# Performance work log

Hardware: AMD Instinct MI355X
Metric: run time of the kernel (lower is better)

The kernel has to match this reference:

```python
import jax, jax.numpy as jnp
import numpy as np
import math

HEADS = 8
KSIZE = 25  # decomposition moving-average window

def moving_avg(x, k):
    # x: [B, S, E]; replicate-pad last axis by (k-1)//2 on both sides, window mean (stride 1)
    p = (k - 1) // 2
    xp = jnp.pad(x, ((0, 0), (0, 0), (p, p)), mode='edge')
    cs = jnp.cumsum(xp, axis=-1)
    cs = jnp.concatenate([jnp.zeros_like(cs[..., :1]), cs], axis=-1)
    return (cs[..., k:] - cs[..., :-k]) / k

def decompose(x, k):
    trend = moving_avg(x, k)
    return x - trend, trend

def setup_inputs() -> dict:
    key = jax.random.key(0)
    ks = jax.random.split(key, 16)
    B, S, E = 4, 2048, 256
    H = HEADS
    D = E // H
    FF = 4 * E
    OUT = E
    s = 0.02
    inp = {
        'x': jax.random.normal(ks[0], (B, S, E), dtype=jnp.float32),
        'mask': jnp.ones((B, 1, 1, S), dtype=jnp.int32),
        'wq': jax.random.normal(ks[1], (D, D), dtype=jnp.float32) * s,
        'wk': jax.random.normal(ks[2], (D, D), dtype=jnp.float32) * s,
        'wv': jax.random.normal(ks[3], (D, D), dtype=jnp.float32) * s,
        'w_out': jax.random.normal(ks[4], (E, E), dtype=jnp.float32) * s,
        'b_out': jnp.zeros((E,), dtype=jnp.float32),
        'ff_w1': jax.random.normal(ks[5], (E, FF), dtype=jnp.float32) * s,
        'ff_b1': jnp.zeros((FF,), dtype=jnp.float32),
        'ff_w2': jax.random.normal(ks[6], (FF, E), dtype=jnp.float32) * s,
        'ff_b2': jnp.zeros((E,), dtype=jnp.float32),
        'pr_w1': jax.random.normal(ks[7], (E, FF), dtype=jnp.float32) * s,
        'pr_b1': jnp.zeros((FF,), dtype=jnp.float32),
        'pr_w2': jax.random.normal(ks[8], (FF, OUT), dtype=jnp.float32) * s,
        'pr_b2': jnp.zeros((OUT,), dtype=jnp.float32),
    }
    return inp

def reference(x, mask, wq, wk, wv, w_out, b_out, ff_w1, ff_b1, ff_w2, ff_b2, pr_w1, pr_b1, pr_w2, pr_b2):
    B, S, E = x.shape
    H = HEADS
    D = E // H
    # multihead attention (per-head shared projections, scale by sqrt(embed_size))
    xh = x.reshape(B, S, H, D)
    q = xh @ wq
    k = xh @ wk
    v = xh @ wv
    scores = jnp.einsum('nqhd,nkhd->nhqk', q, k) / jnp.float32(math.sqrt(E))
    scores = jnp.where(mask == 0, jnp.float32(-1e20), scores)
    attn = jax.nn.softmax(scores, axis=-1)
    attn_out = jnp.einsum('nhqk,nkhd->nqhd', attn, v).reshape(B, S, E)
    attn_out = attn_out @ w_out + b_out
    # residual (dropout is identity at inference)
    x = x + attn_out
    # first decomposition: keep seasonal part
    y, _ = decompose(x, KSIZE)
    # FFN
    z = jnp.maximum(y @ ff_w1 + ff_b1, 0.0) @ ff_w2 + ff_b2
    s = y + z
    # second decomposition
    s, _ = decompose(s, KSIZE)
    # projection FFN
    out = jnp.maximum(s @ pr_w1 + pr_b1, 0.0) @ pr_w2 + pr_b2
    return out
```

## Files before the change

kernel.cpp:

```cpp
#include <hip/hip_runtime.h>
#include <hip/hip_bf16.h>
#include <math.h>

#define B_   4
#define S_   2048
#define E_   256
#define H_   8
#define D_   32
#define FF_  1024
#define NTOK (B_*S_)

typedef __attribute__((ext_vector_type(8))) short short8;
typedef __attribute__((ext_vector_type(4))) float f32x4;
typedef __attribute__((ext_vector_type(4))) unsigned u32x4;
typedef __hip_bfloat16 bf16;

#define QSCALE 0.09016844005556021f

__device__ __forceinline__ unsigned short round_bf16(float a) {
    unsigned ua = __builtin_bit_cast(unsigned, a);
    return (unsigned short)((ua + 0x7fffu + ((ua >> 16) & 1u)) >> 16);
}
__device__ __forceinline__ unsigned cvtpk_bf16(float lo, float hi) {
    unsigned r;
    asm("v_cvt_pk_bf16_f32 %0, %1, %2" : "=v"(r) : "v"(lo), "v"(hi));
    return r;
}
__device__ __forceinline__ float fexp2(float x) {
    float r;
    asm("v_exp_f32 %0, %1" : "=v"(r) : "v"(x));
    return r;
}
__device__ __forceinline__ void gld16(const short* g, short* l) {
    __builtin_amdgcn_global_load_lds(
        (const __attribute__((address_space(1))) unsigned int*)g,
        (__attribute__((address_space(3))) unsigned int*)l, 16, 0, 0);
}
__device__ __forceinline__ short8 lds_frag(const short* base, int r, int c16) {
    return *(const short8*)(base + r*64 + (((c16) ^ (r & 7)) << 3));
}

__global__ __launch_bounds__(256) void qkv_prep_kernel(
    const float* __restrict__ x,
    const float* __restrict__ wq, const float* __restrict__ wk, const float* __restrict__ wv,
    bf16* __restrict__ q, bf16* __restrict__ k, bf16* __restrict__ v,
    const float* __restrict__ w_out, const float* __restrict__ ff_w1,
    const float* __restrict__ ff_w2, const float* __restrict__ pr_w1,
    const float* __restrict__ pr_w2,
    unsigned short* __restrict__ woT, unsigned short* __restrict__ f1T,
    unsigned short* __restrict__ f2T, unsigned short* __restrict__ p1T,
    unsigned short* __restrict__ p2T,
    const int* __restrict__ mask, int* __restrict__ mflags)
{
    const int bid = blockIdx.x;
    if (bid >= 512) {
        const int pb = bid - 512;
        if (pb >= 1088) {
            const int t = threadIdx.x;
            if (t < 128) {
                const int* p = mask + (t >> 5)*S_ + (t & 31)*64;
                int any0 = 0;
                #pragma unroll
                for (int i = 0; i < 16; ++i) {
                    const int4 vv = *(const int4*)(p + i*4);
                    if (!(vv.x && vv.y && vv.z && vv.w)) any0 = 1;
                }
                mflags[t] = any0;
            }
            return;
        }
        const float* w; unsigned short* wt; int K, N, idx;
        if (pb < 64)       { w = w_out; wt = woT; K = E_;  N = E_;  idx = pb; }
        else if (pb < 320) { w = ff_w1; wt = f1T; K = E_;  N = FF_; idx = pb - 64; }
        else if (pb < 576) { w = ff_w2; wt = f2T; K = FF_; N = E_;  idx = pb - 320; }
        else if (pb < 832) { w = pr_w1; wt = p1T; K = E_;  N = FF_; idx = pb - 576; }
        else               { w = pr_w2; wt = p2T; K = FF_; N = E_;  idx = pb - 832; }
        const int nb = N/32;
        const int n0 = (idx % nb)*32, k0 = (idx / nb)*32;
        __shared__ float tile[32][33];
        const int c = threadIdx.x & 31, r0 = threadIdx.x >> 5;
        #pragma unroll
        for (int i = 0; i < 4; ++i)
            tile[r0 + 8*i][c] = w[(size_t)(k0 + r0 + 8*i)*N + n0 + c];
        __syncthreads();
        #pragma unroll
        for (int i = 0; i < 4; ++i)
            wt[(size_t)(n0 + r0 + 8*i)*K + k0 + c] = round_bf16(tile[c][r0 + 8*i]);
        return;
    }
    __shared__ float wqs[D_*D_], wks[D_*D_], wvs[D_*D_];
    __shared__ float xs[16][E_];
    const int tid = threadIdx.x;
    for (int i = tid; i < D_*D_; i += 256) {
        wqs[i] = wq[i]; wks[i] = wk[i]; wvs[i] = wv[i];
    }
    const int tok0 = bid * 16;
    #pragma unroll
    for (int i = 0; i < 16; ++i)
        xs[i][tid] = x[(size_t)(tok0 + i)*E_ + tid];
    __syncthreads();
    const int h = tid >> 5, d = tid & 31;
    for (int t = 0; t < 16; ++t) {
        float aq = 0.f, ak = 0.f, av = 0.f;
        #pragma unroll
        for (int i = 0; i < D_; ++i) {
            const float xv = xs[t][h*D_ + i];
            aq += xv * wqs[i*D_ + d];
            ak += xv * wks[i*D_ + d];
            av += xv * wvs[i*D_ + d];
        }
        const int tok = tok0 + t;
        const int b = tok >> 11;
        const int s = tok & (S_-1);
        const int u = s & 63;
        const int sp = (s & ~63) | (((u>>5)&1)*32 + ((u>>2)&1)*16 + ((u>>3)&3)*4 + (u&3));
        const size_t base = (size_t)(b*H_ + h)*S_;
        q[(base + s )*D_ + d] = __float2bfloat16(aq * QSCALE);
        k[(base + sp)*D_ + d] = __float2bfloat16(ak);
        v[(base + s )*D_ + d] = __float2bfloat16(av);
    }
}

__global__ __launch_bounds__(256) void vtrans_kernel(
    const short* __restrict__ v, short* __restrict__ vt)
{
    __shared__ short t2[D_][256];
    const int tid = threadIdx.x;
    const int bh = blockIdx.x >> 3;
    const int s0 = (blockIdx.x & 7) * 256;
    const short* src = v + ((size_t)bh*S_ + s0 + tid)*D_;
    const short8 r0 = *(const short8*)(src);
    const short8 r1 = *(const short8*)(src + 8);
    const short8 r2 = *(const short8*)(src + 16);
    const short8 r3 = *(const short8*)(src + 24);
    #pragma unroll
    for (int i = 0; i < 8; ++i) {
        t2[i     ][tid] = r0[i];
        t2[i + 8 ][tid] = r1[i];
        t2[i + 16][tid] = r2[i];
        t2[i + 24][tid] = r3[i];
    }
    __syncthreads();
    const int d = tid >> 3, j = tid & 7;
    short* dst = vt + ((size_t)(bh*D_ + d))*S_ + s0 + j*32;
    const short8* row = (const short8*)&t2[d][j*32];
    const short8 o0 = row[0], o1 = row[1], o2 = row[2], o3 = row[3];
    *(short8*)(dst     ) = o0;
    *(short8*)(dst + 8 ) = o1;
    *(short8*)(dst + 16) = o2;
    *(short8*)(dst + 24) = o3;
}

__global__ __launch_bounds__(256) void attn_mfma_kernel(
    const short* __restrict__ qg, const short* __restrict__ kg,
    const short* __restrict__ vtg, const int* __restrict__ mask,
    const int* __restrict__ mflags, unsigned short* __restrict__ attn_out)
{
    __shared__ alignas(16) short lk[2][64*32];
    __shared__ alignas(16) short lv[2][32*64];

    const int tid  = threadIdx.x;
    const int lane = tid & 63;
    const int wid  = tid >> 6;
    const int c    = lane & 15;
    const int g    = lane >> 4;
    const int p    = ((int)blockIdx.x & 7)*64 + ((int)blockIdx.x >> 3);
    const int bh   = p >> 4;
    const int qt   = p & 15;
    const int b    = bh >> 3;
    const int h    = bh & 7;
    const int q0   = qt*128 + wid*32;

    const short* qrow = qg + ((size_t)bh*S_ + q0 + c)*D_ + g*8;
    const short8 qfA = *(const short8*)(qrow);
    const short8 qfB = *(const short8*)(qrow + 16*D_);
    const short* kbase = kg  + (size_t)bh*S_*D_;
    const short* vbase = vtg + (size_t)bh*D_*S_;
    const int*   mrow  = mask + b*S_;

    const int fl = (lane < 32) ? mflags[b*32 + lane] : 0;
    const unsigned long long mbits = __ballot(fl != 0);

    const short* sbase; int soff0, soff1, sinc, dchunk0;
    if (wid < 2) {
        const int R0 = wid*32 + (lane >> 2);
        const int R1 = R0 + 16;
        const int s  = lane & 3;
        soff0 = R0*D_ + ((s ^ ((R0 >> 1) & 3)) << 3);
        soff1 = R1*D_ + ((s ^ ((R1 >> 1) & 3)) << 3);
        sbase = kbase; sinc = 64*D_;
        dchunk0 = wid*1024;
    } else {
        const int r0 = (wid - 2)*16 + (lane >> 3);
        const int r1 = r0 + 8;
        const int s  = lane & 7;
        soff0 = r0*S_ + ((s ^ (r0 & 7)) << 3);
        soff1 = r1*S_ + ((s ^ (r1 & 7)) << 3);
        sbase = vbase; sinc = 64;
        dchunk0 = (wid - 2)*1024;
    }

    const int kaddr = c*D_ + ((g ^ ((c >> 1) & 3)) << 3);
    const int va0   = c*64 + ((g       ^ (c & 7)) << 3);
    const int va1   = c*64 + (((g + 4) ^ (c & 7)) << 3);
    const f32x4 zero = {0.f,0.f,0.f,0.f};
    const short8 ones = { (short)0x3F80, (short)0x3F80, (short)0x3F80, (short)0x3F80,
                          (short)0x3F80, (short)0x3F80, (short)0x3F80, (short)0x3F80 };
    f32x4 oA0 = zero, oA1 = zero, oB0 = zero, oB1 = zero;
    f32x4 lAacc = zero, lBacc = zero;

    {
        short* d0 = (wid < 2 ? &lk[0][0] : &lv[0][0]) + dchunk0;
        gld16(sbase + soff0, d0);
        gld16(sbase + soff1, d0 + 512);
    }
    __syncthreads();

    int buf = 0;
    for (int t = 0; t < 32; ++t) {
        if (t < 31) {
            const short* sp = sbase + (size_t)(t + 1)*sinc;
            short* d0 = (wid < 2 ? &lk[buf ^ 1][0] : &lv[buf ^ 1][0]) + dchunk0;
            gld16(sp + soff0, d0);
            gld16(sp + soff1, d0 + 512);
        }
        const short* LK = &lk[buf][0];
        const short* LV = &lv[buf][0];
        const short8 kf0 = *(const short8*)(LK + kaddr);
        const short8 kf1 = *(const short8*)(LK + kaddr + 512);
        const short8 kf2 = *(const short8*)(LK + kaddr + 1024);
        const short8 kf3 = *(const short8*)(LK + kaddr + 1536);
        __builtin_amdgcn_s_setprio(1);
        f32x4 sA0 = __builtin_amdgcn_mfma_f32_16x16x32_bf16(kf0, qfA, zero, 0, 0, 0);
        f32x4 sA1 = __builtin_amdgcn_mfma_f32_16x16x32_bf16(kf1, qfA, zero, 0, 0, 0);
        f32x4 sA2 = __builtin_amdgcn_mfma_f32_16x16x32_bf16(kf2, qfA, zero, 0, 0, 0);
        f32x4 sA3 = __builtin_amdgcn_mfma_f32_16x16x32_bf16(kf3, qfA, zero, 0, 0, 0);
        f32x4 sB0 = __builtin_amdgcn_mfma_f32_16x16x32_bf16(kf0, qfB, zero, 0, 0, 0);
        f32x4 sB1 = __builtin_amdgcn_mfma_f32_16x16x32_bf16(kf1, qfB, zero, 0, 0, 0);
        f32x4 sB2 = __builtin_amdgcn_mfma_f32_16x16x32_bf16(kf2, qfB, zero, 0, 0, 0);
        f32x4 sB3 = __builtin_amdgcn_mfma_f32_16x16x32_bf16(kf3, qfB, zero, 0, 0, 0);
        __builtin_amdgcn_s_setprio(0);
        if ((mbits >> t) & 1ull) {
            const int kb = t*64 + 8*g;
            #pragma unroll
            for (int r = 0; r < 4; ++r) {
                if (mrow[kb      + r] == 0) { sA0[r] = -1e20f; sB0[r] = -1e20f; }
                if (mrow[kb + 4  + r] == 0) { sA1[r] = -1e20f; sB1[r] = -1e20f; }
                if (mrow[kb + 32 + r] == 0) { sA2[r] = -1e20f; sB2[r] = -1e20f; }
                if (mrow[kb + 36 + r] == 0) { sA3[r] = -1e20f; sB3[r] = -1e20f; }
            }
        }
        f32x4 pA0, pA1, pA2, pA3, pB0, pB1, pB2, pB3;
        #pragma unroll
        for (int r = 0; r < 4; ++r) {
            pA0[r] = fexp2(sA0[r]); pA1[r] = fexp2(sA1[r]);
            pA2[r] = fexp2(sA2[r]); pA3[r] = fexp2(sA3[r]);
            pB0[r] = fexp2(sB0[r]); pB1[r] = fexp2(sB1[r]);
            pB2[r] = fexp2(sB2[r]); pB3[r] = fexp2(sB3[r]);
        }
        const short8 pafA0 = __builtin_bit_cast(short8,
            (u32x4){ cvtpk_bf16(pA0[0],pA0[1]), cvtpk_bf16(pA0[2],pA0[3]),
                     cvtpk_bf16(pA1[0],pA1[1]), cvtpk_bf16(pA1[2],pA1[3]) });
        const short8 pafA1 = __builtin_bit_cast(short8,
            (u32x4){ cvtpk_bf16(pA2[0],pA2[1]), cvtpk_bf16(pA2[2],pA2[3]),
                     cvtpk_bf16(pA3[0],pA3[1]), cvtpk_bf16(pA3[2],pA3[3]) });
        const short8 pafB0 = __builtin_bit_cast(short8,
            (u32x4){ cvtpk_bf16(pB0[0],pB0[1]), cvtpk_bf16(pB0[2],pB0[3]),
                     cvtpk_bf16(pB1[0],pB1[1]), cvtpk_bf16(pB1[2],pB1[3]) });
        const short8 pafB1 = __builtin_bit_cast(short8,
            (u32x4){ cvtpk_bf16(pB2[0],pB2[1]), cvtpk_bf16(pB2[2],pB2[3]),
                     cvtpk_bf16(pB3[0],pB3[1]), cvtpk_bf16(pB3[2],pB3[3]) });
        const short8 vf0 = *(const short8*)(LV + va0);
        const short8 vf1 = *(const short8*)(LV + va1);
        const short8 vf2 = *(const short8*)(LV + va0 + 1024);
        const short8 vf3 = *(const short8*)(LV + va1 + 1024);
        __builtin_amdgcn_s_setprio(1);
        oA0 = __builtin_amdgcn_mfma_f32_16x16x32_bf16(vf0, pafA0, oA0, 0, 0, 0);
        oA0 = __builtin_amdgcn_mfma_f32_16x16x32_bf16(vf1, pafA1, oA0, 0, 0, 0);
        oA1 = __builtin_amdgcn_mfma_f32_16x16x32_bf16(vf2, pafA0, oA1, 0, 0, 0);
        oA1 = __builtin_amdgcn_mfma_f32_16x16x32_bf16(vf3, pafA1, oA1, 0, 0, 0);
        oB0 = __builtin_amdgcn_mfma_f32_16x16x32_bf16(vf0, pafB0, oB0, 0, 0, 0);
        oB0 = __builtin_amdgcn_mfma_f32_16x16x32_bf16(vf1, pafB1, oB0, 0, 0, 0);
        oB1 = __builtin_amdgcn_mfma_f32_16x16x32_bf16(vf2, pafB0, oB1, 0, 0, 0);
        oB1 = __builtin_amdgcn_mfma_f32_16x16x32_bf16(vf3, pafB1, oB1, 0, 0, 0);
        lAacc = __builtin_amdgcn_mfma_f32_16x16x32_bf16(ones, pafA0, lAacc, 0, 0, 0);
        lAacc = __builtin_amdgcn_mfma_f32_16x16x32_bf16(ones, pafA1, lAacc, 0, 0, 0);
        lBacc = __builtin_amdgcn_mfma_f32_16x16x32_bf16(ones, pafB0, lBacc, 0, 0, 0);
        lBacc = __builtin_amdgcn_mfma_f32_16x16x32_bf16(ones, pafB1, lBacc, 0, 0, 0);
        __builtin_amdgcn_s_setprio(0);
        __syncthreads();
        buf ^= 1;
    }
    const float invA = 1.0f / lAacc[0], invB = 1.0f / lBacc[0];
    unsigned short* orowA = attn_out + ((size_t)b*S_ + q0 + c)*E_ + h*D_ + g*4;
    unsigned short* orowB = orowA + (size_t)16*E_;
    uint2 a0, a1, b0, b1;
    a0.x = cvtpk_bf16(oA0[0]*invA, oA0[1]*invA); a0.y = cvtpk_bf16(oA0[2]*invA, oA0[3]*invA);
    a1.x = cvtpk_bf16(oA1[0]*invA, oA1[1]*invA); a1.y = cvtpk_bf16(oA1[2]*invA, oA1[3]*invA);
    b0.x = cvtpk_bf16(oB0[0]*invB, oB0[1]*invB); b0.y = cvtpk_bf16(oB0[2]*invB, oB0[3]*invB);
    b1.x = cvtpk_bf16(oB1[0]*invB, oB1[1]*invB); b1.y = cvtpk_bf16(oB1[2]*invB, oB1[3]*invB);
    *(uint2*)(orowA)      = a0;
    *(uint2*)(orowA + 16) = a1;
    *(uint2*)(orowB)      = b0;
    *(uint2*)(orowB + 16) = b1;
}

template<int BM, int BN, int RELU, int RESID, int WF32, int WBF16>
__global__ __launch_bounds__(256) void mgemm_kernel(
    const short* __restrict__ A, const short* __restrict__ WT,
    const float* __restrict__ bias, const float* __restrict__ R,
    float* __restrict__ C32, unsigned short* __restrict__ Cb,
    int M, int N, int K)
{
    constexpr int FR = BM / 32;
    constexpr int FC = BN / 32;
    __shared__ alignas(16) short As[BM*64];
    __shared__ alignas(16) short Bs[BN*64];
    const int t = threadIdx.x, w = t >> 6, lane = t & 63;
    const int col = lane & 15, grp = lane >> 4;
    const int wm = w >> 1, wn = w & 1;
    const int gx = N / BN;
    const int nwg = gridDim.x;
    const int lin = ((int)blockIdx.x & 7)*(nwg >> 3) + ((int)blockIdx.x >> 3);
    const int bm = lin / gx, bn = lin % gx;
    const int arow = t >> 3, ac = t & 7;

    f32x4 acc[FR][FC];
    #pragma unroll
    for (int i = 0; i < FR; ++i)
        #pragma unroll
        for (int j = 0; j < FC; ++j) acc[i][j] = (f32x4){0.f,0.f,0.f,0.f};

    for (int kb = 0; kb < K; kb += 64) {
        #pragma unroll
        for (int b2 = 0; b2 < BM/32; ++b2) {
            const int row = b2*32 + arow;
            gld16(A + (size_t)(bm*BM + row)*K + kb + ((ac ^ (row & 7)) << 3),
                  As + b2*2048 + w*512);
        }
        #pragma unroll
        for (int b2 = 0; b2 < BN/32; ++b2) {
            const int row = b2*32 + arow;
            gld16(WT + (size_t)(bn*BN + row)*K + kb + ((ac ^ (row & 7)) << 3),
                  Bs + b2*2048 + w*512);
        }
        __syncthreads();
        #pragma unroll
        for (int s = 0; s < 2; ++s) {
            short8 af[FR], bf_[FC];
            #pragma unroll
            for (int fr = 0; fr < FR; ++fr)
                af[fr] = lds_frag(As, wm*(BM/2) + fr*16 + col, s*4 + grp);
            #pragma unroll
            for (int fc = 0; fc < FC; ++fc)
                bf_[fc] = lds_frag(Bs, wn*(BN/2) + fc*16 + col, s*4 + grp);
            #pragma unroll
            for (int fr = 0; fr < FR; ++fr)
                #pragma unroll
                for (int fc = 0; fc < FC; ++fc)
                    acc[fr][fc] = __builtin_amdgcn_mfma_f32_16x16x32_bf16(af[fr], bf_[fc], acc[fr][fc], 0, 0, 0);
        }
        __syncthreads();
    }

    #pragma unroll
    for (int fc = 0; fc < FC; ++fc) {
        const int n = bn*BN + wn*(BN/2) + fc*16 + col;
        const float bs = bias[n];
        #pragma unroll
        for (int fr = 0; fr < FR; ++fr) {
            #pragma unroll
            for (int reg = 0; reg < 4; ++reg) {
                const int m = bm*BM + wm*(BM/2) + fr*16 + grp*4 + reg;
                float v = acc[fr][fc][reg] + bs;
                if (RELU) v = fmaxf(v, 0.f);
                if (RESID) v += R[(size_t)m*N + n];
                if (WF32) C32[(size_t)m*N + n] = v;
                if (WBF16) Cb[(size_t)m*N + n] = round_bf16(v);
            }
        }
    }
}

template<int WF32, int WBF16>
__global__ __launch_bounds__(256) void decomp_kernel(
    const float* __restrict__ in, float* __restrict__ o32, unsigned short* __restrict__ ob)
{
    __shared__ float r[E_];
    const int row = blockIdx.x, e = threadIdx.x;
    const float xv = in[(size_t)row*E_ + e];
    r[e] = xv;
    __syncthreads();
    float sum = 0.f;
    #pragma unroll
    for (int j = -12; j <= 12; ++j) {
        int idx = e + j;
        idx = idx < 0 ? 0 : (idx > E_-1 ? E_-1 : idx);
        sum += r[idx];
    }
    const float res = xv - sum * (1.0f/25.0f);
    if (WF32) o32[(size_t)row*E_ + e] = res;
    if (WBF16) ob[(size_t)row*E_ + e] = round_bf16(res);
}

extern "C" void kernel_launch(void* const* d_in, const int* in_sizes, int n_in,
                              void* d_out, int out_size, void* d_ws, size_t ws_size,
                              hipStream_t stream) {
    const float* x     = (const float*)d_in[0];
    const int*   mask  = (const int*)  d_in[1];
    const float* wq    = (const float*)d_in[2];
    const float* wk    = (const float*)d_in[3];
    const float* wv    = (const float*)d_in[4];
    const float* w_out = (const float*)d_in[5];
    const float* b_out = (const float*)d_in[6];
    const float* ff_w1 = (const float*)d_in[7];
    const float* ff_b1 = (const float*)d_in[8];
    const float* ff_w2 = (const float*)d_in[9];
    const float* ff_b2 = (const float*)d_in[10];
    const float* pr_w1 = (const float*)d_in[11];
    const float* pr_b1 = (const float*)d_in[12];
    const float* pr_w2 = (const float*)d_in[13];
    const float* pr_b2 = (const float*)d_in[14];
    float* out = (float*)d_out;

    char* ws = (char*)d_ws;
    const size_t MB = 1024ull*1024ull;
    const size_t KB = 1024ull;
    bf16*  qb    = (bf16*)(ws + 0*MB);
    bf16*  kbf   = (bf16*)(ws + 4*MB);
    bf16*  vbf   = (bf16*)(ws + 8*MB);
    bf16*  vtb   = (bf16*)(ws + 12*MB);
    unsigned short* attnb = (unsigned short*)(ws + 16*MB);
    float* x1    = (float*)(ws + 20*MB);
    float* y32   = (float*)(ws + 28*MB);
    unsigned short* yb  = (unsigned short*)(ws + 36*MB);
    unsigned short* h1  = (unsigned short*)(ws + 0*MB);
    float* s32   = (float*)(ws + 20*MB);
    unsigned short* s2b = (unsigned short*)(ws + 16*MB);
    unsigned short* h2  = (unsigned short*)(ws + 0*MB);
    unsigned short* woT = (unsigned short*)(ws + 40*MB);
    unsigned short* f1T = (unsigned short*)(ws + 40*MB + 128*KB);
    unsigned short* f2T = (unsigned short*)(ws + 40*MB + 640*KB);
    unsigned short* p1T = (unsigned short*)(ws + 40*MB + 1152*KB);
    unsigned short* p2T = (unsigned short*)(ws + 40*MB + 1664*KB);
    int*            mfl = (int*)           (ws + 40*MB + 2176*KB);

    qkv_prep_kernel<<<1601, 256, 0, stream>>>(x, wq, wk, wv, qb, kbf, vbf,
                                              w_out, ff_w1, ff_w2, pr_w1, pr_w2,
                                              woT, f1T, f2T, p1T, p2T, mask, mfl);
    vtrans_kernel<<<B_*H_*(S_/256), 256, 0, stream>>>((const short*)vbf, (short*)vtb);
    attn_mfma_kernel<<<B_*H_*S_/128, 256, 0, stream>>>(
        (const short*)qb, (const short*)kbf, (const short*)vtb, mask, mfl, attnb);
    mgemm_kernel<64,64,0,1,1,0><<<(NTOK/64)*(E_/64), 256, 0, stream>>>(
        (const short*)attnb, (const short*)woT, b_out, x, x1, nullptr, NTOK, E_, E_);
    decomp_kernel<1,1><<<NTOK, 256, 0, stream>>>(x1, y32, yb);
    mgemm_kernel<128,128,1,0,0,1><<<(NTOK/128)*(FF_/128), 256, 0, stream>>>(
        (const short*)yb, (const short*)f1T, ff_b1, nullptr, nullptr, h1, NTOK, FF_, E_);
    mgemm_kernel<64,64,0,1,1,0><<<(NTOK/64)*(E_/64), 256, 0, stream>>>(
        (const short*)h1, (const short*)f2T, ff_b2, y32, s32, nullptr, NTOK, E_, FF_);
    decomp_kernel<0,1><<<NTOK, 256, 0, stream>>>(s32, nullptr, s2b);
    mgemm_kernel<128,128,1,0,0,1><<<(NTOK/128)*(FF_/128), 256, 0, stream>>>(
        (const short*)s2b, (const short*)p1T, pr_b1, nullptr, nullptr, h2, NTOK, FF_, E_);
    mgemm_kernel<64,64,0,0,1,0><<<(NTOK/64)*(E_/64), 256, 0, stream>>>(
        (const short*)h2, (const short*)p2T, pr_b2, nullptr, out, nullptr, NTOK, E_, FF_);
}
```

Measured before the change: 125.3 us.

## Split attention key range across wave pairs and double-buffer GEMM tiles

The attention kernel now gives each block 64 queries instead of 128 and doubles the grid. Within a block, two wave pairs each cover half of the key sequence, and their partial outputs and row sums are combined through shared memory at the end. This is meant to raise parallelism and shorten the serial key loop, at the cost of more K/V loads per query and an extra reduction step. The GEMM kernel also gains LDS double buffering, so the next k-tile is prefetched while MFMAs run and one barrier per iteration is removed. This doubles its LDS use, which may lower occupancy.

Measured after the change: 132.6 us. 5.8% more time.

```diff
diff --git a/kernel.cpp b/kernel.cpp
--- a/kernel.cpp
+++ b/kernel.cpp
@@ -156,20 +156,22 @@
     const short* __restrict__ vtg, const int* __restrict__ mask,
     const int* __restrict__ mflags, unsigned short* __restrict__ attn_out)
 {
-    __shared__ alignas(16) short lk[2][64*32];
-    __shared__ alignas(16) short lv[2][32*64];
+    __shared__ alignas(16) short lk[2][2][2048];
+    __shared__ alignas(16) short lv[2][2][2048];
 
     const int tid  = threadIdx.x;
     const int lane = tid & 63;
     const int wid  = tid >> 6;
     const int c    = lane & 15;
     const int g    = lane >> 4;
-    const int p    = ((int)blockIdx.x & 7)*64 + ((int)blockIdx.x >> 3);
-    const int bh   = p >> 4;
-    const int qt   = p & 15;
+    const int qs   = wid >> 1;
+    const int half = wid & 1;
+    const int p    = ((int)blockIdx.x & 7)*128 + ((int)blockIdx.x >> 3);
+    const int bh   = p >> 5;
+    const int qt   = p & 31;
     const int b    = bh >> 3;
     const int h    = bh & 7;
-    const int q0   = qt*128 + wid*32;
+    const int q0   = qt*64 + qs*32;
 
     const short* qrow = qg + ((size_t)bh*S_ + q0 + c)*D_ + g*8;
     const short8 qfA = *(const short8*)(qrow);
@@ -181,23 +183,25 @@
     const int fl = (lane < 32) ? mflags[b*32 + lane] : 0;
     const unsigned long long mbits = __ballot(fl != 0);
 
-    const short* sbase; int soff0, soff1, sinc, dchunk0;
-    if (wid < 2) {
-        const int R0 = wid*32 + (lane >> 2);
-        const int R1 = R0 + 16;
-        const int s  = lane & 3;
-        soff0 = R0*D_ + ((s ^ ((R0 >> 1) & 3)) << 3);
-        soff1 = R1*D_ + ((s ^ ((R1 >> 1) & 3)) << 3);
-        sbase = kbase; sinc = 64*D_;
-        dchunk0 = wid*1024;
+    int soff[4]; const short* sgbase; int sinc;
+    if (qs == 0) {
+        const int Rl = lane >> 2, s = lane & 3;
+        #pragma unroll
+        for (int j = 0; j < 4; ++j) {
+            const int R = j*16 + Rl;
+            soff[j] = R*D_ + ((s ^ ((R >> 1) & 3)) << 3);
+        }
+        sgbase = kbase + (size_t)half*16*64*D_;
+        sinc = 64*D_;
     } else {
-        const int r0 = (wid - 2)*16 + (lane >> 3);
-        const int r1 = r0 + 8;
-        const int s  = lane & 7;
-        soff0 = r0*S_ + ((s ^ (r0 & 7)) << 3);
-        soff1 = r1*S_ + ((s ^ (r1 & 7)) << 3);
-        sbase = vbase; sinc = 64;
-        dchunk0 = (wid - 2)*1024;
+        const int rl = lane >> 3, s = lane & 7;
+        #pragma unroll
+        for (int j = 0; j < 4; ++j) {
+            const int r = j*8 + rl;
+            soff[j] = r*S_ + ((s ^ (r & 7)) << 3);
+        }
+        sgbase = vbase + half*16*64;
+        sinc = 64;
     }
 
     const int kaddr = c*D_ + ((g ^ ((c >> 1) & 3)) << 3);
@@ -210,22 +214,22 @@
     f32x4 lAacc = zero, lBacc = zero;
 
     {
-        short* d0 = (wid < 2 ? &lk[0][0] : &lv[0][0]) + dchunk0;
-        gld16(sbase + soff0, d0);
-        gld16(sbase + soff1, d0 + 512);
+        short* d0 = (qs == 0 ? &lk[half][0][0] : &lv[half][0][0]);
+        #pragma unroll
+        for (int j = 0; j < 4; ++j) gld16(sgbase + soff[j], d0 + j*512);
     }
     __syncthreads();
 
     int buf = 0;
-    for (int t = 0; t < 32; ++t) {
-        if (t < 31) {
-            const short* sp = sbase + (size_t)(t + 1)*sinc;
-            short* d0 = (wid < 2 ? &lk[buf ^ 1][0] : &lv[buf ^ 1][0]) + dchunk0;
-            gld16(sp + soff0, d0);
-            gld16(sp + soff1, d0 + 512);
-        }
-        const short* LK = &lk[buf][0];
-        const short* LV = &lv[buf][0];
+    for (int t = 0; t < 16; ++t) {
+        if (t < 15) {
+            const short* sp = sgbase + (size_t)(t + 1)*sinc;
+            short* d0 = (qs == 0 ? &lk[half][buf ^ 1][0] : &lv[half][buf ^ 1][0]);
+            #pragma unroll
+            for (int j = 0; j < 4; ++j) gld16(sp + soff[j], d0 + j*512);
+        }
+        const short* LK = &lk[half][buf][0];
+        const short* LV = &lv[half][buf][0];
         const short8 kf0 = *(const short8*)(LK + kaddr);
         const short8 kf1 = *(const short8*)(LK + kaddr + 512);
         const short8 kf2 = *(const short8*)(LK + kaddr + 1024);
@@ -240,8 +244,9 @@
         f32x4 sB2 = __builtin_amdgcn_mfma_f32_16x16x32_bf16(kf2, qfB, zero, 0, 0, 0);
         f32x4 sB3 = __builtin_amdgcn_mfma_f32_16x16x32_bf16(kf3, qfB, zero, 0, 0, 0);
         __builtin_amdgcn_s_setprio(0);
-        if ((mbits >> t) & 1ull) {
-            const int kb = t*64 + 8*g;
+        const int tt = half*16 + t;
+        if ((mbits >> tt) & 1ull) {
+            const int kb = tt*64 + 8*g;
             #pragma unroll
             for (int r = 0; r < 4; ++r) {
                 if (mrow[kb      + r] == 0) { sA0[r] = -1e20f; sB0[r] = -1e20f; }
@@ -291,18 +296,39 @@
         __syncthreads();
         buf ^= 1;
     }
-    const float invA = 1.0f / lAacc[0], invB = 1.0f / lBacc[0];
-    unsigned short* orowA = attn_out + ((size_t)b*S_ + q0 + c)*E_ + h*D_ + g*4;
-    unsigned short* orowB = orowA + (size_t)16*E_;
-    uint2 a0, a1, b0, b1;
-    a0.x = cvtpk_bf16(oA0[0]*invA, oA0[1]*invA); a0.y = cvtpk_bf16(oA0[2]*invA, oA0[3]*invA);
-    a1.x = cvtpk_bf16(oA1[0]*invA, oA1[1]*invA); a1.y = cvtpk_bf16(oA1[2]*invA, oA1[3]*invA);
-    b0.x = cvtpk_bf16(oB0[0]*invB, oB0[1]*invB); b0.y = cvtpk_bf16(oB0[2]*invB, oB0[3]*invB);
-    b1.x = cvtpk_bf16(oB1[0]*invB, oB1[1]*invB); b1.y = cvtpk_bf16(oB1[2]*invB, oB1[3]*invB);
-    *(uint2*)(orowA)      = a0;
-    *(uint2*)(orowA + 16) = a1;
-    *(uint2*)(orowB)      = b0;
-    *(uint2*)(orowB + 16) = b1;
+    float* oM = (float*)&lk[0][0][0];
+    float* lM = (float*)&lv[0][0][0];
+    if (half == 1) {
+        float* o = oM + (qs*64 + lane)*16;
+        #pragma unroll
+        for (int r = 0; r < 4; ++r) {
+            o[r] = oA0[r]; o[4 + r] = oA1[r]; o[8 + r] = oB0[r]; o[12 + r] = oB1[r];
+        }
+        lM[(qs*64 + lane)*2 + 0] = lAacc[0];
+        lM[(qs*64 + lane)*2 + 1] = lBacc[0];
+    }
+    __syncthreads();
+    if (half == 0) {
+        const float* o = oM + (qs*64 + lane)*16;
+        const float lA = lAacc[0] + lM[(qs*64 + lane)*2 + 0];
+        const float lB = lBacc[0] + lM[(qs*64 + lane)*2 + 1];
+        const float invA = 1.0f / lA, invB = 1.0f / lB;
+        unsigned short* orowA = attn_out + ((size_t)b*S_ + q0 + c)*E_ + h*D_ + g*4;
+        unsigned short* orowB = orowA + (size_t)16*E_;
+        uint2 a0, a1, b0, b1;
+        a0.x = cvtpk_bf16((oA0[0]+o[0])*invA,  (oA0[1]+o[1])*invA);
+        a0.y = cvtpk_bf16((oA0[2]+o[2])*invA,  (oA0[3]+o[3])*invA);
+        a1.x = cvtpk_bf16((oA1[0]+o[4])*invA,  (oA1[1]+o[5])*invA);
+        a1.y = cvtpk_bf16((oA1[2]+o[6])*invA,  (oA1[3]+o[7])*invA);
+        b0.x = cvtpk_bf16((oB0[0]+o[8])*invB,  (oB0[1]+o[9])*invB);
+        b0.y = cvtpk_bf16((oB0[2]+o[10])*invB, (oB0[3]+o[11])*invB);
+        b1.x = cvtpk_bf16((oB1[0]+o[12])*invB, (oB1[1]+o[13])*invB);
+        b1.y = cvtpk_bf16((oB1[2]+o[14])*invB, (oB1[3]+o[15])*invB);
+        *(uint2*)(orowA)      = a0;
+        *(uint2*)(orowA + 16) = a1;
+        *(uint2*)(orowB)      = b0;
+        *(uint2*)(orowB + 16) = b1;
+    }
 }
 
 template<int BM, int BN, int RELU, int RESID, int WF32, int WBF16>
@@ -314,8 +340,8 @@
 {
     constexpr int FR = BM / 32;
     constexpr int FC = BN / 32;
-    __shared__ alignas(16) short As[BM*64];
-    __shared__ alignas(16) short Bs[BN*64];
+    __shared__ alignas(16) short As[2][BM*64];
+    __shared__ alignas(16) short Bs[2][BN*64];
     const int t = threadIdx.x, w = t >> 6, lane = t & 63;
     const int col = lane & 15, grp = lane >> 4;
     const int wm = w >> 1, wn = w & 1;
@@ -331,36 +357,55 @@
         #pragma unroll
         for (int j = 0; j < FC; ++j) acc[i][j] = (f32x4){0.f,0.f,0.f,0.f};
 
+    #pragma unroll
+    for (int b2 = 0; b2 < BM/32; ++b2) {
+        const int row = b2*32 + arow;
+        gld16(A + (size_t)(bm*BM + row)*K + ((ac ^ (row & 7)) << 3),
+              &As[0][0] + b2*2048 + w*512);
+    }
+    #pragma unroll
+    for (int b2 = 0; b2 < BN/32; ++b2) {
+        const int row = b2*32 + arow;
+        gld16(WT + (size_t)(bn*BN + row)*K + ((ac ^ (row & 7)) << 3),
+              &Bs[0][0] + b2*2048 + w*512);
+    }
+    __syncthreads();
+
+    int buf = 0;
     for (int kb = 0; kb < K; kb += 64) {
-        #pragma unroll
-        for (int b2 = 0; b2 < BM/32; ++b2) {
-            const int row = b2*32 + arow;
-            gld16(A + (size_t)(bm*BM + row)*K + kb + ((ac ^ (row & 7)) << 3),
-                  As + b2*2048 + w*512);
-        }
-        #pragma unroll
-        for (int b2 = 0; b2 < BN/32; ++b2) {
-            const int row = b2*32 + arow;
-            gld16(WT + (size_t)(bn*BN + row)*K + kb + ((ac ^ (row & 7)) << 3),
-                  Bs + b2*2048 + w*512);
-        }
-        __syncthreads();
+        if (kb + 64 < K) {
+            #pragma unroll
+            for (int b2 = 0; b2 < BM/32; ++b2) {
+                const int row = b2*32 + arow;
+                gld16(A + (size_t)(bm*BM + row)*K + kb + 64 + ((ac ^ (row & 7)) << 3),
+                      &As[buf ^ 1][0] + b2*2048 + w*512);
+            }
+            #pragma unroll
+            for (int b2 = 0; b2 < BN/32; ++b2) {
+                const int row = b2*32 + arow;
+                gld16(WT + (size_t)(bn*BN + row)*K + kb + 64 + ((ac ^ (row & 7)) << 3),
+                      &Bs[buf ^ 1][0] + b2*2048 + w*512);
+            }
+        }
         #pragma unroll
         for (int s = 0; s < 2; ++s) {
             short8 af[FR], bf_[FC];
             #pragma unroll
             for (int fr = 0; fr < FR; ++fr)
-                af[fr] = lds_frag(As, wm*(BM/2) + fr*16 + col, s*4 + grp);
+                af[fr] = lds_frag(&As[buf][0], wm*(BM/2) + fr*16 + col, s*4 + grp);
             #pragma unroll
             for (int fc = 0; fc < FC; ++fc)
-                bf_[fc] = lds_frag(Bs, wn*(BN/2) + fc*16 + col, s*4 + grp);
+                bf_[fc] = lds_frag(&Bs[buf][0], wn*(BN/2) + fc*16 + col, s*4 + grp);
+            __builtin_amdgcn_s_setprio(1);
             #pragma unroll
             for (int fr = 0; fr < FR; ++fr)
                 #pragma unroll
                 for (int fc = 0; fc < FC; ++fc)
                     acc[fr][fc] = __builtin_amdgcn_mfma_f32_16x16x32_bf16(af[fr], bf_[fc], acc[fr][fc], 0, 0, 0);
+            __builtin_amdgcn_s_setprio(0);
         }
         __syncthreads();
+        buf ^= 1;
     }
 
     #pragma unroll
@@ -449,7 +494,7 @@
                                               w_out, ff_w1, ff_w2, pr_w1, pr_w2,
                                               woT, f1T, f2T, p1T, p2T, mask, mfl);
     vtrans_kernel<<<B_*H_*(S_/256), 256, 0, stream>>>((const short*)vbf, (short*)vtb);
-    attn_mfma_kernel<<<B_*H_*S_/128, 256, 0, stream>>>(
+    attn_mfma_kernel<<<B_*H_*S_/64, 256, 0, stream>>>(
         (const short*)qb, (const short*)kbf, (const short*)vtb, mask, mfl, attnb);
     mgemm_kernel<64,64,0,1,1,0><<<(NTOK/64)*(E_/64), 256, 0, stream>>>(
         (const short*)attnb, (const short*)woT, b_out, x, x1, nullptr, NTOK, E_, E_);
```
